# Kernel optimization log

Hardware: AMD Instinct MI355X
Metric: run time of the kernel (lower is better)

## Reference

```python
import jax, jax.numpy as jnp
import numpy as np

B, N, D = 4, 4096, 1024
STD = 1.0 / D

def setup_inputs() -> dict:
    key = jax.random.key(0)
    ks = jax.random.split(key, 6)
    return {
        "x_real": jax.random.normal(ks[0], (B, N, D), dtype=jnp.float32),
        "x_imag": jax.random.normal(ks[1], (B, N, D), dtype=jnp.float32),
        "w_query_real": jax.random.normal(ks[2], (D, D), dtype=jnp.float32) * STD,
        "w_query_imag": jax.random.normal(ks[3], (D, D), dtype=jnp.float32) * STD,
        "w_key": jax.random.normal(ks[4], (D, D), dtype=jnp.float32) * STD,
        "w_value": jax.random.normal(ks[5], (D, D), dtype=jnp.float32) * STD,
    }

def reference(x_real, x_imag, w_query_real, w_query_imag, w_key, w_value):
    # query gate: (x.real @ Wqr) * (x.imag @ Wqi)  -> [b, n, e]
    query = jnp.einsum('bnd,de->bne', x_real, w_query_real) * \
            jnp.einsum('bnd,de->bne', x_imag, w_query_imag)
    key = jnp.einsum('bnd,de->bne', x_real, w_key)      # [b, n, d]
    value = jnp.einsum('bnd,de->bne', x_imag, w_value)  # [b, n, e]
    # linear-attention style reduction over sequence dim n
    kv_attn = jnp.einsum('bnd,bne->bde', key, value)    # [b, d, e]
    # dropout with p=0.0 (eval / identity)
    bffn = jnp.einsum('bnd,bde->bne', query, kv_attn)   # [b, n, e]
    return bffn
```

## Files before the change

### kernel.cpp

```cpp
#include <hip/hip_runtime.h>
#include <stdint.h>

typedef unsigned short ushort_t;
typedef __attribute__((ext_vector_type(8))) short bf16x8;
typedef __attribute__((ext_vector_type(4))) float f32x4;

__device__ __forceinline__ ushort_t f2bf(float f) {
  union { float f; uint32_t u; } v; v.f = f;
  uint32_t u = v.u;
  u += 0x7FFFu + ((u >> 16) & 1u);
  return (ushort_t)(u >> 16);
}
__device__ __forceinline__ float bf2f(ushort_t h) {
  union { uint32_t u; float f; } v; v.u = ((uint32_t)h) << 16;
  return v.f;
}
__device__ __forceinline__ void gl2lds16(const void* g, void* l) {
  __builtin_amdgcn_global_load_lds(
      (__attribute__((address_space(1))) void*)(uintptr_t)g,
      (__attribute__((address_space(3))) void*)(uint32_t)(uintptr_t)l,
      16, 0, 0);
}

__device__ __forceinline__ void gemm_loop(
    const ushort_t* __restrict__ A, int lda,
    const ushort_t* __restrict__ Bt, int ldb,
    int m0, int n0, int K,
    ushort_t* __restrict__ As, ushort_t* __restrict__ Bs,
    f32x4 (&acc)[4][4]) {
  const int t = threadIdx.x;
  const int lane = t & 63, wid = t >> 6;
  const int wm = wid & 1, wn = wid >> 1;
  const int lr = lane & 15, lq = lane >> 4;

  const ushort_t* ap[4];
  const ushort_t* bp[4];
  int dst[4];
  #pragma unroll
  for (int i = 0; i < 4; ++i) {
    int slot = i * 256 + t;
    int row = slot >> 3, kgp = slot & 7;
    int kg = kgp ^ (row & 7);
    dst[i] = slot * 16;
    ap[i] = A + (size_t)(m0 + row) * lda + kg * 8;
    bp[i] = Bt + (size_t)(n0 + row) * ldb + kg * 8;
  }

  int aoff[2][4], boff[2][4];
  #pragma unroll
  for (int s = 0; s < 2; ++s)
    #pragma unroll
    for (int i = 0; i < 4; ++i) {
      int ra = wm * 64 + i * 16 + lr;
      aoff[s][i] = ra * 128 + (((s * 4 + lq) ^ (ra & 7)) * 16);
      int rb = wn * 64 + i * 16 + lr;
      boff[s][i] = rb * 128 + (((s * 4 + lq) ^ (rb & 7)) * 16);
    }

  for (int k0 = 0; k0 < K; k0 += 64) {
    #pragma unroll
    for (int i = 0; i < 4; ++i) gl2lds16(bp[i] + k0, (char*)Bs + dst[i]);
    #pragma unroll
    for (int i = 0; i < 4; ++i) gl2lds16(ap[i] + k0, (char*)As + dst[i]);
    __syncthreads();
    #pragma unroll
    for (int s = 0; s < 2; ++s) {
      bf16x8 af[4], bfr[4];
      #pragma unroll
      for (int i = 0; i < 4; ++i) af[i] = *(const bf16x8*)((const char*)As + aoff[s][i]);
      #pragma unroll
      for (int i = 0; i < 4; ++i) bfr[i] = *(const bf16x8*)((const char*)Bs + boff[s][i]);
      #pragma unroll
      for (int mi = 0; mi < 4; ++mi)
        #pragma unroll
        for (int ni = 0; ni < 4; ++ni)
          acc[mi][ni] = __builtin_amdgcn_mfma_f32_16x16x32_bf16(af[mi], bfr[ni], acc[mi][ni], 0, 0, 0);
    }
    __syncthreads();
  }
}

template <bool GATE>
__global__ __launch_bounds__(256) void proj_gemm(
    const ushort_t* __restrict__ X, const ushort_t* __restrict__ Wt,
    ushort_t* __restrict__ Cq, ushort_t* __restrict__ Ct,
    const ushort_t* __restrict__ gate) {
  __shared__ ushort_t As[128 * 64];
  __shared__ ushort_t Bs[128 * 64];
  const int bid = blockIdx.x;
  const int xcd = bid & 7, i = bid >> 3;
  const int m0 = (xcd * 16 + (i >> 4)) * 128;
  const int n0 = (i & 15) * 128;
  f32x4 acc[4][4] = {};
  gemm_loop(X, 1024, Wt, 1024, m0, n0, 1024, As, Bs, acc);

  const int t = threadIdx.x, lane = t & 63, wid = t >> 6;
  const int wm = wid & 1, wn = wid >> 1;
  const int lr = lane & 15, lq = lane >> 4;

  if (n0 < 1024) {
    #pragma unroll
    for (int mi = 0; mi < 4; ++mi) {
      int rbase = m0 + wm * 64 + mi * 16 + lq * 4;
      #pragma unroll
      for (int ni = 0; ni < 4; ++ni) {
        int c = n0 + wn * 64 + ni * 16 + lr;
        #pragma unroll
        for (int r = 0; r < 4; ++r) {
          float v = acc[mi][ni][r];
          if constexpr (GATE) v *= bf2f(gate[(size_t)(rbase + r) * 1024 + c]);
          Cq[(size_t)(rbase + r) * 1024 + c] = f2bf(v);
        }
      }
    }
  } else {
    #pragma unroll
    for (int mi = 0; mi < 4; ++mi) {
      int m = m0 + wm * 64 + mi * 16 + lq * 4;
      int b = m >> 12, nseq = m & 4095;
      #pragma unroll
      for (int ni = 0; ni < 4; ++ni) {
        int d = n0 - 1024 + wn * 64 + ni * 16 + lr;
        ushort4 u = make_ushort4(f2bf(acc[mi][ni][0]), f2bf(acc[mi][ni][1]),
                                 f2bf(acc[mi][ni][2]), f2bf(acc[mi][ni][3]));
        *(ushort4*)&Ct[((size_t)(b * 1024 + d) << 12) + nseq] = u;
      }
    }
  }
}

__global__ __launch_bounds__(256) void kv_gemm(
    const ushort_t* __restrict__ VT, const ushort_t* __restrict__ KT,
    float* __restrict__ P) {
  __shared__ ushort_t As[128 * 64];
  __shared__ ushort_t Bs[128 * 64];
  const int bid = blockIdx.x;
  const int xcd = bid & 7, i = bid >> 3;
  const int z = xcd * 2 + (i >> 6);
  const int mn = i & 63;
  const int m0 = (mn >> 3) * 128, n0 = (mn & 7) * 128;
  const int b = z & 3, s = z >> 2;
  const ushort_t* A = VT + ((size_t)b << 22) + s * 1024;
  const ushort_t* Bt = KT + ((size_t)b << 22) + s * 1024;
  f32x4 acc[4][4] = {};
  gemm_loop(A, 4096, Bt, 4096, m0, n0, 1024, As, Bs, acc);

  const int t = threadIdx.x, lane = t & 63, wid = t >> 6;
  const int wm = wid & 1, wn = wid >> 1;
  const int lr = lane & 15, lq = lane >> 4;
  float* C = P + ((size_t)z << 20);
  #pragma unroll
  for (int mi = 0; mi < 4; ++mi) {
    int rbase = m0 + wm * 64 + mi * 16 + lq * 4;
    #pragma unroll
    for (int ni = 0; ni < 4; ++ni) {
      int c = n0 + wn * 64 + ni * 16 + lr;
      #pragma unroll
      for (int r = 0; r < 4; ++r)
        C[(size_t)(rbase + r) * 1024 + c] = acc[mi][ni][r];
    }
  }
}

__global__ __launch_bounds__(256) void kv_reduce(const float* __restrict__ P,
                                                 ushort_t* __restrict__ KVT) {
  size_t e4 = ((size_t)blockIdx.x * 256 + threadIdx.x) * 4;
  int b = (int)(e4 >> 20);
  size_t j = e4 & ((1u << 20) - 1);
  float4 s = make_float4(0.f, 0.f, 0.f, 0.f);
  #pragma unroll
  for (int sp = 0; sp < 4; ++sp) {
    float4 v = *(const float4*)(P + ((size_t)(sp * 4 + b) << 20) + j);
    s.x += v.x; s.y += v.y; s.z += v.z; s.w += v.w;
  }
  *(ushort4*)&KVT[e4] = make_ushort4(f2bf(s.x), f2bf(s.y), f2bf(s.z), f2bf(s.w));
}

__global__ __launch_bounds__(256) void fin_gemm(
    const ushort_t* __restrict__ Q, const ushort_t* __restrict__ KVT,
    float* __restrict__ Out) {
  __shared__ ushort_t As[128 * 64];
  __shared__ ushort_t Bs[128 * 64];
  const int bid = blockIdx.x;
  const int xcd = bid & 7, i = bid >> 3;
  const int m0 = (xcd * 16 + (i >> 3)) * 128;
  const int n0 = (i & 7) * 128;
  const int b = m0 >> 12;
  f32x4 acc[4][4] = {};
  gemm_loop(Q, 1024, KVT + ((size_t)b << 20), 1024, m0, n0, 1024, As, Bs, acc);

  const int t = threadIdx.x, lane = t & 63, wid = t >> 6;
  const int wm = wid & 1, wn = wid >> 1;
  const int lr = lane & 15, lq = lane >> 4;
  #pragma unroll
  for (int mi = 0; mi < 4; ++mi) {
    int rbase = m0 + wm * 64 + mi * 16 + lq * 4;
    #pragma unroll
    for (int ni = 0; ni < 4; ++ni) {
      int c = n0 + wn * 64 + ni * 16 + lr;
      #pragma unroll
      for (int r = 0; r < 4; ++r)
        Out[(size_t)(rbase + r) * 1024 + c] = acc[mi][ni][r];
    }
  }
}

__global__ __launch_bounds__(256) void wtrans4(
    const float* w0, const float* w1, const float* w2, const float* w3,
    ushort_t* o0, ushort_t* o1, ushort_t* o2, ushort_t* o3) {
  __shared__ float tile[32][33];
  const float* W; ushort_t* O;
  switch (blockIdx.z) {
    case 0: W = w0; O = o0; break;
    case 1: W = w1; O = o1; break;
    case 2: W = w2; O = o2; break;
    default: W = w3; O = o3; break;
  }
  const int tx = threadIdx.x, ty = threadIdx.y;
  const int bx = blockIdx.x * 32, by = blockIdx.y * 32;
  #pragma unroll
  for (int k = 0; k < 32; k += 8)
    tile[ty + k][tx] = W[(size_t)(by + ty + k) * 1024 + bx + tx];
  __syncthreads();
  #pragma unroll
  for (int k = 0; k < 32; k += 8)
    O[(size_t)(bx + ty + k) * 1024 + by + tx] = f2bf(tile[tx][ty + k]);
}

__global__ __launch_bounds__(256) void xconvert(
    const float* __restrict__ xr, const float* __restrict__ xi,
    ushort_t* __restrict__ xrb, ushort_t* __restrict__ xib) {
  const size_t T = 16u * 1024u * 1024u;
  size_t e = ((size_t)blockIdx.x * 256 + threadIdx.x) * 8;
  const float* src; ushort_t* dst;
  if (e < T) { src = xr + e; dst = xrb + e; }
  else       { src = xi + (e - T); dst = xib + (e - T); }
  float4 f0 = *(const float4*)src;
  float4 f1 = *(const float4*)(src + 4);
  ushort4 u0 = make_ushort4(f2bf(f0.x), f2bf(f0.y), f2bf(f0.z), f2bf(f0.w));
  ushort4 u1 = make_ushort4(f2bf(f1.x), f2bf(f1.y), f2bf(f1.z), f2bf(f1.w));
  *(ushort4*)dst = u0;
  *(ushort4*)(dst + 4) = u1;
}

extern "C" void kernel_launch(void* const* d_in, const int* in_sizes, int n_in,
                              void* d_out, int out_size, void* d_ws, size_t ws_size,
                              hipStream_t stream) {
  const float* xr  = (const float*)d_in[0];
  const float* xi  = (const float*)d_in[1];
  const float* wqr = (const float*)d_in[2];
  const float* wqi = (const float*)d_in[3];
  const float* wk  = (const float*)d_in[4];
  const float* wv  = (const float*)d_in[5];

  char* ws = (char*)d_ws;
  const size_t MB = 1024ull * 1024ull;
  ushort_t* WtQR = (ushort_t*)(ws + 0 * MB);
  ushort_t* WtK  = (ushort_t*)(ws + 2 * MB);
  ushort_t* WtQI = (ushort_t*)(ws + 4 * MB);
  ushort_t* WtV  = (ushort_t*)(ws + 6 * MB);
  ushort_t* Xrb  = (ushort_t*)(ws + 8 * MB);
  ushort_t* Xib  = (ushort_t*)(ws + 40 * MB);
  ushort_t* KT   = (ushort_t*)(ws + 72 * MB);
  ushort_t* Q    = (ushort_t*)(ws + 104 * MB);
  ushort_t* VT   = (ushort_t*)(ws + 8 * MB);
  ushort_t* KVT  = (ushort_t*)(ws + 40 * MB);
  ushort_t* QR   = (ushort_t*)d_out;
  float*    KVP  = (float*)d_out;

  wtrans4<<<dim3(32, 32, 4), dim3(32, 8), 0, stream>>>(wqr, wk, wqi, wv,
                                                       WtQR, WtK, WtQI, WtV);
  xconvert<<<16384, 256, 0, stream>>>(xr, xi, Xrb, Xib);
  proj_gemm<false><<<2048, 256, 0, stream>>>(Xrb, WtQR, QR, KT, nullptr);
  proj_gemm<true><<<2048, 256, 0, stream>>>(Xib, WtQI, Q, VT, QR);
  kv_gemm<<<1024, 256, 0, stream>>>(VT, KT, KVP);
  kv_reduce<<<4096, 256, 0, stream>>>(KVP, KVT);
  fin_gemm<<<1024, 256, 0, stream>>>(Q, KVT, (float*)d_out);
}
```

Measured before the change: 439.3 us.

## Stage transposed projection stores through LDS, store KV split-K partials as bf16, merge prep kernels

The K/V-transposed epilogue of proj_gemm now writes the tile into swizzled shared memory and then emits 16-byte coalesced row stores, replacing scattered 8-byte writes along the sequence dimension. The kv_gemm split-K partials are stored as bf16 instead of fp32, halving the write and reread traffic in kv_reduce at the cost of extra rounding before the sum. The weight transpose and x conversion kernels are merged into one launch to remove a launch boundary.

```diff
diff --git a/kernel.cpp b/kernel.cpp
--- a/kernel.cpp
+++ b/kernel.cpp
@@ -85,8 +85,9 @@
     const ushort_t* __restrict__ X, const ushort_t* __restrict__ Wt,
     ushort_t* __restrict__ Cq, ushort_t* __restrict__ Ct,
     const ushort_t* __restrict__ gate) {
-  __shared__ ushort_t As[128 * 64];
-  __shared__ ushort_t Bs[128 * 64];
+  __shared__ ushort_t smem[2 * 128 * 64];
+  ushort_t* As = smem;
+  ushort_t* Bs = smem + 128 * 64;
   const int bid = blockIdx.x;
   const int xcd = bid & 7, i = bid >> 3;
   const int m0 = (xcd * 16 + (i >> 4)) * 128;
@@ -116,24 +117,35 @@
   } else {
     #pragma unroll
     for (int mi = 0; mi < 4; ++mi) {
-      int m = m0 + wm * 64 + mi * 16 + lq * 4;
-      int b = m >> 12, nseq = m & 4095;
+      int ns = wm * 64 + mi * 16 + lq * 4;
+      int nc = ns >> 3, half = (ns >> 2) & 1;
       #pragma unroll
       for (int ni = 0; ni < 4; ++ni) {
-        int d = n0 - 1024 + wn * 64 + ni * 16 + lr;
+        int dl = wn * 64 + ni * 16 + lr;
         ushort4 u = make_ushort4(f2bf(acc[mi][ni][0]), f2bf(acc[mi][ni][1]),
                                  f2bf(acc[mi][ni][2]), f2bf(acc[mi][ni][3]));
-        *(ushort4*)&Ct[((size_t)(b * 1024 + d) << 12) + nseq] = u;
+        *(ushort4*)((char*)smem + dl * 256 + ((nc ^ (dl & 15)) * 16) + half * 8) = u;
       }
+    }
+    __syncthreads();
+    const int b = m0 >> 12, nseq0 = m0 & 4095;
+    #pragma unroll
+    for (int j = 0; j < 8; ++j) {
+      int g = j * 256 + t;
+      int dl = g >> 4, nc = g & 15;
+      bf16x8 v = *(const bf16x8*)((const char*)smem + dl * 256 + ((nc ^ (dl & 15)) * 16));
+      int d = n0 - 1024 + dl;
+      *(bf16x8*)&Ct[(((size_t)(b * 1024 + d)) << 12) + nseq0 + nc * 8] = v;
     }
   }
 }
 
 __global__ __launch_bounds__(256) void kv_gemm(
     const ushort_t* __restrict__ VT, const ushort_t* __restrict__ KT,
-    float* __restrict__ P) {
-  __shared__ ushort_t As[128 * 64];
-  __shared__ ushort_t Bs[128 * 64];
+    ushort_t* __restrict__ P) {
+  __shared__ ushort_t smem[2 * 128 * 64];
+  ushort_t* As = smem;
+  ushort_t* Bs = smem + 128 * 64;
   const int bid = blockIdx.x;
   const int xcd = bid & 7, i = bid >> 3;
   const int z = xcd * 2 + (i >> 6);
@@ -148,7 +160,7 @@
   const int t = threadIdx.x, lane = t & 63, wid = t >> 6;
   const int wm = wid & 1, wn = wid >> 1;
   const int lr = lane & 15, lq = lane >> 4;
-  float* C = P + ((size_t)z << 20);
+  ushort_t* C = P + ((size_t)z << 20);
   #pragma unroll
   for (int mi = 0; mi < 4; ++mi) {
     int rbase = m0 + wm * 64 + mi * 16 + lq * 4;
@@ -157,30 +169,31 @@
       int c = n0 + wn * 64 + ni * 16 + lr;
       #pragma unroll
       for (int r = 0; r < 4; ++r)
-        C[(size_t)(rbase + r) * 1024 + c] = acc[mi][ni][r];
-    }
-  }
-}
-
-__global__ __launch_bounds__(256) void kv_reduce(const float* __restrict__ P,
+        C[(size_t)(rbase + r) * 1024 + c] = f2bf(acc[mi][ni][r]);
+    }
+  }
+}
+
+__global__ __launch_bounds__(256) void kv_reduce(const ushort_t* __restrict__ P,
                                                  ushort_t* __restrict__ KVT) {
   size_t e4 = ((size_t)blockIdx.x * 256 + threadIdx.x) * 4;
   int b = (int)(e4 >> 20);
   size_t j = e4 & ((1u << 20) - 1);
-  float4 s = make_float4(0.f, 0.f, 0.f, 0.f);
+  float s0 = 0.f, s1 = 0.f, s2 = 0.f, s3 = 0.f;
   #pragma unroll
   for (int sp = 0; sp < 4; ++sp) {
-    float4 v = *(const float4*)(P + ((size_t)(sp * 4 + b) << 20) + j);
-    s.x += v.x; s.y += v.y; s.z += v.z; s.w += v.w;
-  }
-  *(ushort4*)&KVT[e4] = make_ushort4(f2bf(s.x), f2bf(s.y), f2bf(s.z), f2bf(s.w));
+    ushort4 v = *(const ushort4*)(P + ((size_t)(sp * 4 + b) << 20) + j);
+    s0 += bf2f(v.x); s1 += bf2f(v.y); s2 += bf2f(v.z); s3 += bf2f(v.w);
+  }
+  *(ushort4*)&KVT[e4] = make_ushort4(f2bf(s0), f2bf(s1), f2bf(s2), f2bf(s3));
 }
 
 __global__ __launch_bounds__(256) void fin_gemm(
     const ushort_t* __restrict__ Q, const ushort_t* __restrict__ KVT,
     float* __restrict__ Out) {
-  __shared__ ushort_t As[128 * 64];
-  __shared__ ushort_t Bs[128 * 64];
+  __shared__ ushort_t smem[2 * 128 * 64];
+  ushort_t* As = smem;
+  ushort_t* Bs = smem + 128 * 64;
   const int bid = blockIdx.x;
   const int xcd = bid & 7, i = bid >> 3;
   const int m0 = (xcd * 16 + (i >> 3)) * 128;
@@ -205,42 +218,45 @@
   }
 }
 
-__global__ __launch_bounds__(256) void wtrans4(
+__global__ __launch_bounds__(256) void prep(
+    const float* __restrict__ xr, const float* __restrict__ xi,
     const float* w0, const float* w1, const float* w2, const float* w3,
+    ushort_t* __restrict__ xrb, ushort_t* __restrict__ xib,
     ushort_t* o0, ushort_t* o1, ushort_t* o2, ushort_t* o3) {
-  __shared__ float tile[32][33];
-  const float* W; ushort_t* O;
-  switch (blockIdx.z) {
-    case 0: W = w0; O = o0; break;
-    case 1: W = w1; O = o1; break;
-    case 2: W = w2; O = o2; break;
-    default: W = w3; O = o3; break;
-  }
-  const int tx = threadIdx.x, ty = threadIdx.y;
-  const int bx = blockIdx.x * 32, by = blockIdx.y * 32;
-  #pragma unroll
-  for (int k = 0; k < 32; k += 8)
-    tile[ty + k][tx] = W[(size_t)(by + ty + k) * 1024 + bx + tx];
-  __syncthreads();
-  #pragma unroll
-  for (int k = 0; k < 32; k += 8)
-    O[(size_t)(bx + ty + k) * 1024 + by + tx] = f2bf(tile[tx][ty + k]);
-}
-
-__global__ __launch_bounds__(256) void xconvert(
-    const float* __restrict__ xr, const float* __restrict__ xi,
-    ushort_t* __restrict__ xrb, ushort_t* __restrict__ xib) {
-  const size_t T = 16u * 1024u * 1024u;
-  size_t e = ((size_t)blockIdx.x * 256 + threadIdx.x) * 8;
-  const float* src; ushort_t* dst;
-  if (e < T) { src = xr + e; dst = xrb + e; }
-  else       { src = xi + (e - T); dst = xib + (e - T); }
-  float4 f0 = *(const float4*)src;
-  float4 f1 = *(const float4*)(src + 4);
-  ushort4 u0 = make_ushort4(f2bf(f0.x), f2bf(f0.y), f2bf(f0.z), f2bf(f0.w));
-  ushort4 u1 = make_ushort4(f2bf(f1.x), f2bf(f1.y), f2bf(f1.z), f2bf(f1.w));
-  *(ushort4*)dst = u0;
-  *(ushort4*)(dst + 4) = u1;
+  const int bid = blockIdx.x;
+  const int t = threadIdx.x;
+  if (bid < 4096) {
+    __shared__ float tile[32][33];
+    const float* W; ushort_t* O;
+    switch (bid >> 10) {
+      case 0: W = w0; O = o0; break;
+      case 1: W = w1; O = o1; break;
+      case 2: W = w2; O = o2; break;
+      default: W = w3; O = o3; break;
+    }
+    const int within = bid & 1023;
+    const int bx = (within & 31) * 32, by = (within >> 5) * 32;
+    const int tx = t & 31, ty = t >> 5;
+    #pragma unroll
+    for (int k = 0; k < 32; k += 8)
+      tile[ty + k][tx] = W[(size_t)(by + ty + k) * 1024 + bx + tx];
+    __syncthreads();
+    #pragma unroll
+    for (int k = 0; k < 32; k += 8)
+      O[(size_t)(bx + ty + k) * 1024 + by + tx] = f2bf(tile[tx][ty + k]);
+  } else {
+    const size_t T = 16u * 1024u * 1024u;
+    size_t e = ((size_t)(bid - 4096) * 256 + t) * 8;
+    const float* src; ushort_t* dst;
+    if (e < T) { src = xr + e; dst = xrb + e; }
+    else       { src = xi + (e - T); dst = xib + (e - T); }
+    float4 f0 = *(const float4*)src;
+    float4 f1 = *(const float4*)(src + 4);
+    ushort4 u0 = make_ushort4(f2bf(f0.x), f2bf(f0.y), f2bf(f0.z), f2bf(f0.w));
+    ushort4 u1 = make_ushort4(f2bf(f1.x), f2bf(f1.y), f2bf(f1.z), f2bf(f1.w));
+    *(ushort4*)dst = u0;
+    *(ushort4*)(dst + 4) = u1;
+  }
 }
 
 extern "C" void kernel_launch(void* const* d_in, const int* in_sizes, int n_in,
@@ -266,11 +282,10 @@
   ushort_t* VT   = (ushort_t*)(ws + 8 * MB);
   ushort_t* KVT  = (ushort_t*)(ws + 40 * MB);
   ushort_t* QR   = (ushort_t*)d_out;
-  float*    KVP  = (float*)d_out;
-
-  wtrans4<<<dim3(32, 32, 4), dim3(32, 8), 0, stream>>>(wqr, wk, wqi, wv,
-                                                       WtQR, WtK, WtQI, WtV);
-  xconvert<<<16384, 256, 0, stream>>>(xr, xi, Xrb, Xib);
+  ushort_t* KVP  = (ushort_t*)d_out;
+
+  prep<<<20480, 256, 0, stream>>>(xr, xi, wqr, wqi, wk, wv,
+                                  Xrb, Xib, WtQR, WtQI, WtK, WtV);
   proj_gemm<false><<<2048, 256, 0, stream>>>(Xrb, WtQR, QR, KT, nullptr);
   proj_gemm<true><<<2048, 256, 0, stream>>>(Xib, WtQI, Q, VT, QR);
   kv_gemm<<<1024, 256, 0, stream>>>(VT, KT, KVP);
```

Measured after the change: 429.0 us. 2.3% less time.
